# Kernel tuning notes

Measured on AMD Instinct MI355X. Metric: run time of the kernel, lower is better.

Reference implementation:

```python
import jax, jax.numpy as jnp
import numpy as np

LEAKY_SLOPE = 0.2

def _xavier(key, shape, gain=1.414):
    a = gain * np.sqrt(6.0 / (shape[0] + shape[1]))
    return jax.random.uniform(key, shape, minval=-a, maxval=a, dtype=jnp.float32)

C_IN, HID = 64, 128
S_SCALES = [25, 12, 5]
T_SCALES = [64, 32, 16]

def setup_inputs() -> dict:
    key = jax.random.key(0)
    ks = jax.random.split(key, 32)
    B, T, J = 256, 64, 25
    d = {}
    d["src"] = jax.random.normal(ks[0], (B, C_IN, T, J), dtype=jnp.float32)
    d["W"] = _xavier(ks[1], (C_IN, HID))
    for i in range(3):
        d[f"as_src{i}"] = _xavier(ks[2 + i], (HID, 1))
        d[f"as_dst{i}"] = _xavier(ks[5 + i], (HID, 1))
        d[f"at_src{i}"] = _xavier(ks[8 + i], (HID, 1))
        d[f"at_dst{i}"] = _xavier(ks[11 + i], (HID, 1))
    # DiffPool assignment linears: in_features -> next_scale
    d["Wsp0"] = _xavier(ks[14], (C_IN, S_SCALES[1])); d["bsp0"] = jnp.zeros((S_SCALES[1],), jnp.float32)
    d["Wsp1"] = _xavier(ks[15], (C_IN, S_SCALES[2])); d["bsp1"] = jnp.zeros((S_SCALES[2],), jnp.float32)
    d["Wtp0"] = _xavier(ks[16], (C_IN, T_SCALES[1])); d["btp0"] = jnp.zeros((T_SCALES[1],), jnp.float32)
    d["Wtp1"] = _xavier(ks[17], (C_IN, T_SCALES[2])); d["btp1"] = jnp.zeros((T_SCALES[2],), jnp.float32)
    return d


def _gat_attn(emb, a_src, a_dst):
    # emb: [N, n, H]; additive GAT scores -> [N, n, n]
    s = emb @ a_src            # [N, n, 1]
    t = emb @ a_dst            # [N, n, 1]
    return jax.nn.leaky_relu(s + jnp.swapaxes(t, -1, -2), LEAKY_SLOPE)


def _diffpool(x, attn, Wp, bp):
    # assignment S = softmax(Linear(A @ X)) : [N, n, n_next]
    S = jax.nn.softmax((attn @ x) @ Wp + bp, axis=-1)
    x_next = jnp.einsum('bnk,bnc->bkc', S, x)
    return x_next, S


def _branch(x0, W, a_srcs, a_dsts, pool_params):
    n_scales = len(a_srcs)
    attns, pools = [], []
    x_cur = x0
    for i in range(n_scales):
        emb = x_cur @ W
        attns.append(_gat_attn(emb, a_srcs[i], a_dsts[i]))
        if i < n_scales - 1:
            Wp, bp = pool_params[i]
            x_cur, S = _diffpool(x_cur, attns[i], Wp, bp)
            pools.append(S)
    fusion = attns[0]
    for i in range(1, n_scales):
        S = pools[0]
        for j in range(1, i):
            S = S @ pools[j]
        fusion = fusion + S @ attns[i] @ jnp.swapaxes(S, -1, -2)
    # dropout is identity in eval mode
    return jax.nn.softmax(fusion, axis=-1)


def reference(src, W, as_src0, as_src1, as_src2, as_dst0, as_dst1, as_dst2,
              at_src0, at_src1, at_src2, at_dst0, at_dst1, at_dst2,
              Wsp0, bsp0, Wsp1, bsp1, Wtp0, btp0, Wtp1, btp1):
    B, C_in, T, J = src.shape
    x = jnp.transpose(src, (0, 2, 3, 1))              # [B, T, J, C]
    sp_x = x.reshape(B * T, J, C_in)                   # spatial graphs
    tp_x = jnp.transpose(x, (0, 2, 1, 3)).reshape(B * J, T, C_in)  # temporal graphs

    sa = _branch(sp_x, W, [as_src0, as_src1, as_src2], [as_dst0, as_dst1, as_dst2],
                 [(Wsp0, bsp0), (Wsp1, bsp1)])
    ta = _branch(tp_x, W, [at_src0, at_src1, at_src2], [at_dst0, at_dst1, at_dst2],
                 [(Wtp0, btp0), (Wtp1, btp1)])
    return sa.reshape(B, T, J, J), ta.reshape(B, J, T, T)
```

## Files before the change

### kernel.cpp

```cpp
#include <hip/hip_runtime.h>
#include <math.h>

constexpr float LEAKY = 0.2f;

__device__ __forceinline__ float4 ldf4(const float* p){ return *reinterpret_cast<const float4*>(p); }
__device__ __forceinline__ void stf4(float* p, float4 v){ *reinterpret_cast<float4*>(p) = v; }
__device__ __forceinline__ float dot4(float4 a, float4 b){ return a.x*b.x + a.y*b.y + a.z*b.z + a.w*b.w; }
__device__ __forceinline__ float4 fma4(float s, float4 b, float4 acc){
    acc.x += s*b.x; acc.y += s*b.y; acc.z += s*b.z; acc.w += s*b.w; return acc;
}
__device__ __forceinline__ float lrelu(float f){ return f > 0.f ? f : LEAKY*f; }
__device__ __forceinline__ float4 lrelu4(float s, float4 t){
    float4 r; r.x = lrelu(s+t.x); r.y = lrelu(s+t.y); r.z = lrelu(s+t.z); r.w = lrelu(s+t.w); return r;
}
__device__ __forceinline__ float vmax4(float4 v){ return fmaxf(fmaxf(v.x,v.y), fmaxf(v.z,v.w)); }
__device__ __forceinline__ float vsum4(float4 v){ return v.x+v.y+v.z+v.w; }
__device__ __forceinline__ float4 exp4(float4 a, float mx){
    float4 r; r.x = __expf(a.x-mx); r.y = __expf(a.y-mx); r.z = __expf(a.z-mx); r.w = __expf(a.w-mx); return r;
}

__global__ void prep_kernel(const float* __restrict__ W,
    const float* a0, const float* a1, const float* a2,  const float* a3,
    const float* a4, const float* a5, const float* a6,  const float* a7,
    const float* a8, const float* a9, const float* a10, const float* a11,
    const float* __restrict__ Wsp0, const float* __restrict__ Wsp1,
    const float* __restrict__ Wtp0, const float* __restrict__ Wtp1,
    float* __restrict__ ws)
{
    int blk = blockIdx.x, t = threadIdx.x;
    if (blk < 12) {
        const float* as[12] = {a0,a1,a2,a3,a4,a5,a6,a7,a8,a9,a10,a11};
        const float* a = as[blk];
        float s = 0.f;
        #pragma unroll
        for (int h = 0; h < 128; ++h) s += W[t*128 + h] * a[h];
        ws[blk*64 + t] = s;
    } else if (blk == 12) {
        for (int i = t; i < 768; i += 64) { int k = i >> 6, c = i & 63; ws[768 + i] = Wsp0[c*12 + k]; }
    } else if (blk == 13) {
        for (int i = t; i < 320; i += 64) { int k = i >> 6, c = i & 63; ws[1536 + i] = Wsp1[c*5 + k]; }
    } else if (blk == 14) {
        for (int i = t; i < 2048; i += 64) { int k = i >> 6, c = i & 63; ws[1856 + i] = Wtp0[c*32 + k]; }
    } else {
        for (int i = t; i < 1024; i += 64) { int k = i >> 6, c = i & 63; ws[3904 + i] = Wtp1[c*16 + k]; }
    }
}

__global__ __launch_bounds__(512, 4)
void temporal_kernel(const float* __restrict__ src, const float* __restrict__ wvec_g,
                     const float* __restrict__ Wp0, const float* __restrict__ b0,
                     const float* __restrict__ Wp1, const float* __restrict__ b1,
                     float* __restrict__ out, int nwg8)
{
    constexpr int NT = 512;
    constexpr int oA1 = 0;
    constexpr int oP1 = 1152;
    constexpr int oS1 = 1792;

    __shared__ __align__(16) float xr[4352];
    __shared__ __align__(16) float A0[4352];
    __shared__ __align__(16) float PR[2304];
    __shared__ __align__(16) float S0[2304];
    __shared__ __align__(16) float sv[64], tv[64], rx[64], rs[64];
    __shared__ __align__(16) float wv[384];

    const int tid = threadIdx.x;
    const int g = (blockIdx.x & 7) * nwg8 + (blockIdx.x >> 3);
    const int b = g / 25, inner = g - b*25;

    for (int i = tid; i < 384; i += NT) wv[i] = wvec_g[i];
    for (int i = tid; i < 4096; i += NT) {
        int c = i >> 6, r = i & 63;
        xr[r*68 + c] = src[((size_t)(b*64 + c)*64 + r)*25 + inner];
    }
    __syncthreads();

    for (int i = tid; i < 128; i += NT) {
        int which = i >> 6, p = i & 63;
        const float* w = wv + which*64;
        float acc = 0.f;
        #pragma unroll
        for (int c = 0; c < 64; c += 4) acc += dot4(ldf4(&xr[p*68 + c]), ldf4(&w[c]));
        if (which) tv[p] = acc; else sv[p] = acc;
    }
    for (int i = tid; i < 512; i += NT) {
        int p = i >> 3, k4 = i & 7;
        float4 acc = {0,0,0,0};
        #pragma unroll
        for (int c = 0; c < 64; ++c) acc = fma4(xr[p*68 + c], ldf4(&Wp0[c*32 + 4*k4]), acc);
        stf4(&PR[p*36 + 4*k4], acc);
    }
    __syncthreads();

    for (int i = tid; i < 1024; i += NT) {
        int p = i >> 4, q4 = i & 15;
        stf4(&A0[p*68 + 4*q4], lrelu4(sv[p], ldf4(&tv[4*q4])));
    }
    __syncthreads();

    if (tid < 256) {
        int p = tid >> 2, k8 = tid & 3;
        float4 acc0 = ldf4(&b0[8*k8]);
        float4 acc1 = ldf4(&b0[8*k8 + 4]);
        #pragma unroll
        for (int m = 0; m < 64; ++m) {
            float a = A0[p*68 + m];
            acc0 = fma4(a, ldf4(&PR[m*36 + 8*k8]), acc0);
            acc1 = fma4(a, ldf4(&PR[m*36 + 8*k8 + 4]), acc1);
        }
        stf4(&S0[p*36 + 8*k8], acc0);
        stf4(&S0[p*36 + 8*k8 + 4], acc1);
    }
    __syncthreads();

    {
        int p = tid >> 3, l = tid & 7;
        float4 v = ldf4(&S0[p*36 + 4*l]);
        float mx = vmax4(v);
        mx = fmaxf(mx, __shfl_xor(mx,1)); mx = fmaxf(mx, __shfl_xor(mx,2)); mx = fmaxf(mx, __shfl_xor(mx,4));
        v = exp4(v, mx);
        float sm = vsum4(v);
        sm += __shfl_xor(sm,1); sm += __shfl_xor(sm,2); sm += __shfl_xor(sm,4);
        float inv = 1.f/sm;
        v.x *= inv; v.y *= inv; v.z *= inv; v.w *= inv;
        stf4(&S0[p*36 + 4*l], v);
    }
    __syncthreads();

    if (tid < 256) {
        int k = tid >> 3, c8 = tid & 7;
        float4 acc0 = {0,0,0,0}, acc1 = {0,0,0,0};
        #pragma unroll
        for (int p = 0; p < 64; ++p) {
            float s = S0[p*36 + k];
            acc0 = fma4(s, ldf4(&xr[p*68 + 8*c8]), acc0);
            acc1 = fma4(s, ldf4(&xr[p*68 + 8*c8 + 4]), acc1);
        }
        stf4(&PR[k*68 + 8*c8], acc0);
        stf4(&PR[k*68 + 8*c8 + 4], acc1);
    }
    __syncthreads();

    for (int i = tid; i < 64; i += NT) {
        int which = i >> 5, p = i & 31;
        const float* w = wv + (2 + which)*64;
        float acc = 0.f;
        #pragma unroll
        for (int c = 0; c < 64; c += 4) acc += dot4(ldf4(&PR[p*68 + c]), ldf4(&w[c]));
        if (which) tv[p] = acc; else sv[p] = acc;
    }
    for (int i = tid; i < 128; i += NT) {
        int p = i >> 2, k4 = i & 3;
        float4 acc = {0,0,0,0};
        #pragma unroll
        for (int c = 0; c < 64; ++c) acc = fma4(PR[p*68 + c], ldf4(&Wp1[c*16 + 4*k4]), acc);
        stf4(&xr[oP1 + p*20 + 4*k4], acc);
    }
    __syncthreads();

    for (int i = tid; i < 1024; i += NT) {
        int p = i >> 5, q = i & 31;
        xr[oA1 + p*36 + q] = lrelu(sv[p] + tv[q]);
    }
    __syncthreads();

    for (int i = tid; i < 128; i += NT) {
        int p = i >> 2, k4 = i & 3;
        float4 acc = ldf4(&b1[4*k4]);
        #pragma unroll
        for (int m = 0; m < 32; ++m) acc = fma4(xr[oA1 + p*36 + m], ldf4(&xr[oP1 + m*20 + 4*k4]), acc);
        stf4(&xr[oS1 + p*20 + 4*k4], acc);
    }
    __syncthreads();

    if (tid < 128) {
        int m = tid >> 2, l = tid & 3;
        float4 v = ldf4(&xr[oS1 + m*20 + 4*l]);
        float mx = vmax4(v);
        mx = fmaxf(mx, __shfl_xor(mx,1)); mx = fmaxf(mx, __shfl_xor(mx,2));
        v = exp4(v, mx);
        float sm = vsum4(v);
        sm += __shfl_xor(sm,1); sm += __shfl_xor(sm,2);
        float inv = 1.f/sm;
        v.x *= inv; v.y *= inv; v.z *= inv; v.w *= inv;
        stf4(&xr[oS1 + m*20 + 4*l], v);
    } else if (tid < 192) {
        int i = tid - 128;
        int which = i >> 5, p = i & 31;
        const float* w = wv + (4 + which)*64;
        float acc = 0.f;
        #pragma unroll
        for (int c = 0; c < 64; c += 4) acc += dot4(ldf4(&PR[p*68 + c]), ldf4(&w[c]));
        if (which) tv[p] = acc; else sv[p] = acc;
    }
    __syncthreads();

    for (int k = tid; k < 16; k += NT) {
        float a = 0.f, c2 = 0.f;
        #pragma unroll
        for (int n = 0; n < 32; ++n) { float s1 = xr[oS1 + n*20 + k]; a += s1*sv[n]; c2 += s1*tv[n]; }
        rx[k] = a; rs[k] = c2;
    }
    __syncthreads();

    {
        int m = tid >> 4, k = tid & 15;
        float rsk = rs[k];
        float acc = 0.f;
        #pragma unroll
        for (int j = 0; j < 16; ++j)
            acc += xr[oS1 + m*20 + j] * lrelu(rx[j] + rsk);
        xr[oP1 + m*20 + k] = acc;
    }
    __syncthreads();

    for (int i = tid; i < 1024; i += NT) {
        int m = i >> 5, n = i & 31;
        float acc = xr[oA1 + m*36 + n];
        #pragma unroll
        for (int j4 = 0; j4 < 4; ++j4)
            acc += dot4(ldf4(&xr[oP1 + m*20 + 4*j4]), ldf4(&xr[oS1 + n*20 + 4*j4]));
        xr[oA1 + m*36 + n] = acc;
    }
    __syncthreads();

    for (int i = tid; i < 512; i += NT) {
        int p = i >> 3, k4 = i & 7;
        float4 acc = {0,0,0,0};
        #pragma unroll
        for (int m = 0; m < 32; ++m) acc = fma4(S0[p*36 + m], ldf4(&xr[oA1 + m*36 + 4*k4]), acc);
        stf4(&PR[p*36 + 4*k4], acc);
    }
    __syncthreads();

    {
        int q = tid & 63, pg = tid >> 6;
        float4 s0r[8];
        #pragma unroll
        for (int j = 0; j < 8; ++j) s0r[j] = ldf4(&S0[q*36 + 4*j]);
        #pragma unroll
        for (int pi = 0; pi < 8; ++pi) {
            int p = pg*8 + pi;
            float acc = 0.f;
            #pragma unroll
            for (int j = 0; j < 8; ++j) acc += dot4(ldf4(&PR[p*36 + 4*j]), s0r[j]);
            A0[p*68 + q] += acc;
        }
    }
    __syncthreads();

    {
        int p = tid >> 3, l = tid & 7;
        float4 v1 = ldf4(&A0[p*68 + 4*l]);
        float4 v2 = ldf4(&A0[p*68 + 32 + 4*l]);
        float mx = fmaxf(vmax4(v1), vmax4(v2));
        mx = fmaxf(mx, __shfl_xor(mx,1)); mx = fmaxf(mx, __shfl_xor(mx,2)); mx = fmaxf(mx, __shfl_xor(mx,4));
        float4 e1 = exp4(v1, mx), e2 = exp4(v2, mx);
        float sm = vsum4(e1) + vsum4(e2);
        sm += __shfl_xor(sm,1); sm += __shfl_xor(sm,2); sm += __shfl_xor(sm,4);
        float inv = 1.f/sm;
        e1.x*=inv; e1.y*=inv; e1.z*=inv; e1.w*=inv;
        e2.x*=inv; e2.y*=inv; e2.z*=inv; e2.w*=inv;
        size_t base = (size_t)g*4096 + (size_t)p*64;
        stf4(&out[base + 4*l], e1);
        stf4(&out[base + 32 + 4*l], e2);
    }
}

__global__ __launch_bounds__(256, 4)
void spatial_kernel(const float* __restrict__ src, const float* __restrict__ wvg,
                    const float* __restrict__ WpT0, const float* __restrict__ WpT1,
                    const float* __restrict__ b0, const float* __restrict__ b1,
                    float* __restrict__ out, int nwg8)
{
    __shared__ __align__(16) float Rx0[1700];
    __shared__ __align__(16) float RA0[700];
    __shared__ __align__(16) float RPR[816];
    __shared__ __align__(16) float RS0[500];
    __shared__ __align__(16) float sv[32], tv[32], ua[32], va[32], rxa[8], rsa[8];

    float* x0  = Rx0;
    float* A1  = Rx0;
    float* A1T = Rx0 + 240;
    float* P1T = Rx0 + 480;
    float* S1  = Rx0 + 540;
    float* S1T = Rx0 + 684;
    float* A2T = Rx0 + 744;
    float* S01 = Rx0 + 804;
    float* A0  = RA0;
    float* P0T = RPR;
    float* x1  = RPR;
    float* M1  = RPR;
    float* M2  = RPR;
    float* S0  = RS0;

    const int t = threadIdx.x;
    const int g = (blockIdx.x & 7) * nwg8 + (blockIdx.x >> 3);
    const int b = g >> 6, inner = g & 63;
    const float* srcb = src + (size_t)b*102400 + inner*25;

    for (int i = t; i < 400; i += 256) {
        int r = i % 25, c0 = (i / 25) << 2;
        float4 v;
        v.x = srcb[(c0+0)*1600 + r];
        v.y = srcb[(c0+1)*1600 + r];
        v.z = srcb[(c0+2)*1600 + r];
        v.w = srcb[(c0+3)*1600 + r];
        stf4(&x0[r*68 + c0], v);
    }
    __syncthreads();

    if (t < 50) {
        int which = t / 25, p = t - which*25;
        const float* w = wvg + which*64;
        float a = 0.f;
        #pragma unroll
        for (int c4 = 0; c4 < 16; ++c4) a += dot4(ldf4(&x0[p*68 + 4*c4]), ldf4(&w[4*c4]));
        if (which) tv[p] = a; else sv[p] = a;
    }
    for (int i = t; i < 336; i += 256) {
        int k = i / 28, m = i - k*28;
        float a = 0.f;
        if (m < 25) {
            #pragma unroll
            for (int c4 = 0; c4 < 16; ++c4) a += dot4(ldf4(&WpT0[k*64 + 4*c4]), ldf4(&x0[m*68 + 4*c4]));
        }
        P0T[k*28 + m] = a;
    }
    __syncthreads();

    for (int i = t; i < 700; i += 256) {
        int p = i / 28, q = i - p*28;
        A0[i] = (q < 25) ? lrelu(sv[p] + tv[q]) : -1e30f;
    }
    __syncthreads();

    for (int i = t; i < 300; i += 256) {
        int p = i / 12, k = i - p*12;
        float acc = b0[k];
        #pragma unroll
        for (int m4 = 0; m4 < 7; ++m4) acc += dot4(ldf4(&A0[p*28 + 4*m4]), ldf4(&P0T[k*28 + 4*m4]));
        S0[p*20 + k] = acc;
    }
    __syncthreads();

    if (t < 25) {
        float4 r[3]; float mx = -1e30f;
        #pragma unroll
        for (int u = 0; u < 3; ++u) { r[u] = ldf4(&S0[t*20 + 4*u]); mx = fmaxf(mx, vmax4(r[u])); }
        float sm = 0.f;
        #pragma unroll
        for (int u = 0; u < 3; ++u) { r[u] = exp4(r[u], mx); sm += vsum4(r[u]); }
        float inv = 1.f/sm;
        #pragma unroll
        for (int u = 0; u < 3; ++u) {
            r[u].x *= inv; r[u].y *= inv; r[u].z *= inv; r[u].w *= inv;
            stf4(&S0[t*20 + 4*u], r[u]);
        }
    }
    __syncthreads();

    if (t < 96) {
        int k = t >> 3, c0 = (t & 7) << 3;
        float4 a = {0,0,0,0}, bb = {0,0,0,0};
        #pragma unroll
        for (int p = 0; p < 25; ++p) {
            float s = S0[p*20 + k];
            a  = fma4(s, ldf4(&x0[p*68 + c0]), a);
            bb = fma4(s, ldf4(&x0[p*68 + c0 + 4]), bb);
        }
        stf4(&x1[k*68 + c0], a);
        stf4(&x1[k*68 + c0 + 4], bb);
    }
    __syncthreads();

    if (t < 48) {
        int which = t / 12, p = t - which*12;
        const float* w = wvg + (2+which)*64;
        float a = 0.f;
        #pragma unroll
        for (int c4 = 0; c4 < 16; ++c4) a += dot4(ldf4(&x1[p*68 + 4*c4]), ldf4(&w[4*c4]));
        if (which == 0) sv[p] = a; else if (which == 1) tv[p] = a;
        else if (which == 2) ua[p] = a; else va[p] = a;
    }
    for (int i = t; i < 60; i += 256) {
        int j = i / 12, k = i - j*12;
        float a = 0.f;
        #pragma unroll
        for (int c4 = 0; c4 < 16; ++c4) a += dot4(ldf4(&WpT1[j*64 + 4*c4]), ldf4(&x1[k*68 + 4*c4]));
        P1T[j*12 + k] = a;
    }
    __syncthreads();

    for (int i = t; i < 288; i += 256) {
        int mat = i / 144, rr = (i - mat*144) / 12, q = i % 12;
        if (mat == 0) A1 [rr*20 + q] = lrelu(sv[rr] + tv[q]);
        else          A1T[rr*20 + q] = lrelu(sv[q] + tv[rr]);
    }
    __syncthreads();

    for (int i = t; i < 300; i += 256) {
        int p = i / 12, k = i - p*12;
        float acc = 0.f;
        #pragma unroll
        for (int m4 = 0; m4 < 3; ++m4) acc += dot4(ldf4(&S0[p*20 + 4*m4]), ldf4(&A1T[k*20 + 4*m4]));
        M1[p*20 + k] = acc;
    }
    for (int i = t; i < 60; i += 256) {
        int m = i / 5, j = i - m*5;
        float acc = b1[j];
        #pragma unroll
        for (int k4 = 0; k4 < 3; ++k4) acc += dot4(ldf4(&A1[m*20 + 4*k4]), ldf4(&P1T[j*12 + 4*k4]));
        S1[m*12 + j] = acc;
    }
    __syncthreads();

    if (t < 12) {
        float mx = -1e30f;
        float r0 = S1[t*12+0], r1 = S1[t*12+1], r2 = S1[t*12+2], r3 = S1[t*12+3], r4 = S1[t*12+4];
        mx = fmaxf(fmaxf(fmaxf(r0,r1), fmaxf(r2,r3)), r4);
        r0 = __expf(r0-mx); r1 = __expf(r1-mx); r2 = __expf(r2-mx); r3 = __expf(r3-mx); r4 = __expf(r4-mx);
        float inv = 1.f/(r0+r1+r2+r3+r4);
        S1[t*12+0] = r0*inv; S1[t*12+1] = r1*inv; S1[t*12+2] = r2*inv; S1[t*12+3] = r3*inv; S1[t*12+4] = r4*inv;
    }
    for (int i = t; i < 625; i += 256) {
        int p = i / 25, q = i - p*25;
        float acc = A0[p*28 + q];
        #pragma unroll
        for (int m4 = 0; m4 < 3; ++m4) acc += dot4(ldf4(&M1[p*20 + 4*m4]), ldf4(&S0[q*20 + 4*m4]));
        A0[p*28 + q] = acc;
    }
    __syncthreads();

    for (int i = t; i < 60; i += 256) {
        int j = i / 12, m = i - j*12;
        S1T[j*12 + m] = S1[m*12 + j];
    }
    if (t >= 64 && t < 74) {
        int tp = t - 64, which = tp / 5, k = tp - which*5;
        float a = 0.f;
        #pragma unroll
        for (int n = 0; n < 12; ++n) a += S1[n*12 + k] * (which ? va[n] : ua[n]);
        if (which) rsa[k] = a; else rxa[k] = a;
    }
    __syncthreads();

    for (int i = t; i < 40; i += 256) {
        int q = i >> 3, p = i & 7;
        A2T[q*12 + p] = (p < 5) ? lrelu(rxa[p] + rsa[q]) : 0.f;
    }
    for (int i = t; i < 200; i += 256) {
        int p = i >> 3, c = i & 7;
        float acc = 0.f;
        if (c < 5) {
            #pragma unroll
            for (int m4 = 0; m4 < 3; ++m4) acc += dot4(ldf4(&S0[p*20 + 4*m4]), ldf4(&S1T[c*12 + 4*m4]));
        }
        S01[p*12 + c] = acc;
    }
    __syncthreads();

    for (int i = t; i < 200; i += 256) {
        int p = i >> 3, k = i & 7;
        float acc = 0.f;
        if (k < 5) {
            #pragma unroll
            for (int m4 = 0; m4 < 2; ++m4) acc += dot4(ldf4(&S01[p*12 + 4*m4]), ldf4(&A2T[k*12 + 4*m4]));
        }
        M2[p*12 + k] = acc;
    }
    __syncthreads();

    for (int i = t; i < 625; i += 256) {
        int p = i / 25, q = i - p*25;
        float acc = A0[p*28 + q];
        #pragma unroll
        for (int m4 = 0; m4 < 2; ++m4) acc += dot4(ldf4(&M2[p*12 + 4*m4]), ldf4(&S01[q*12 + 4*m4]));
        A0[p*28 + q] = acc;
    }
    __syncthreads();

    if (t < 25) {
        float4 r[7]; float mx = -1e30f;
        #pragma unroll
        for (int u = 0; u < 7; ++u) { r[u] = ldf4(&A0[t*28 + 4*u]); mx = fmaxf(mx, vmax4(r[u])); }
        float sm = 0.f;
        #pragma unroll
        for (int u = 0; u < 7; ++u) sm += vsum4(exp4(r[u], mx));
        sv[t] = mx; tv[t] = 1.f/sm;
    }
    __syncthreads();

    for (int i = t; i < 625; i += 256) {
        int p = i / 25, q = i - p*25;
        out[(size_t)g*625 + i] = __expf(A0[p*28 + q] - sv[p]) * tv[p];
    }
}

extern "C" void kernel_launch(void* const* d_in, const int* in_sizes, int n_in,
                              void* d_out, int out_size, void* d_ws, size_t ws_size,
                              hipStream_t stream) {
    const float* src = (const float*)d_in[0];
    const float* W   = (const float*)d_in[1];
    float* ws = (float*)d_ws;

    prep_kernel<<<16, 64, 0, stream>>>(W,
        (const float*)d_in[2],  (const float*)d_in[3],
        (const float*)d_in[6],  (const float*)d_in[7],
        (const float*)d_in[10], (const float*)d_in[11],
        (const float*)d_in[4],  (const float*)d_in[5],
        (const float*)d_in[8],  (const float*)d_in[9],
        (const float*)d_in[12], (const float*)d_in[13],
        (const float*)d_in[14], (const float*)d_in[16],
        (const float*)d_in[18], (const float*)d_in[20],
        ws);

    float* out = (float*)d_out;
    spatial_kernel<<<16384, 256, 0, stream>>>(
        src, ws, ws + 768, ws + 1536,
        (const float*)d_in[15], (const float*)d_in[17],
        out, 16384/8);
    temporal_kernel<<<6400, 512, 0, stream>>>(
        src, ws + 384,
        (const float*)d_in[18], (const float*)d_in[19],
        (const float*)d_in[20], (const float*)d_in[21],
        out + 10240000, 6400/8);
}
```

Measured before the change: 482.8 us.

## Reassociate pooled projections and fold scale-2 attention into scale-1 term

In the temporal kernel, the pooled-feature products (S^T X)·W and (S^T X)·Wp1 are reassociated as S^T·(X·W) and S^T·(X·Wp1), so the 32x64 pooled feature matrix is never built. The S0 matmul is also register-blocked to two rows per thread. In the spatial kernel, the scale-2 contribution S1·A2·S1^T is added into A1 before projecting through S0, which removes the S01/M2 passes and one 625-element accumulation sweep. These changes cut arithmetic and shared-memory traffic, at the cost of extra shared buffers, added barriers in the spatial path, and slightly different floating-point rounding.

```diff
diff --git a/kernel.cpp b/kernel.cpp
--- a/kernel.cpp
+++ b/kernel.cpp
@@ -61,7 +61,10 @@
     __shared__ __align__(16) float A0[4352];
     __shared__ __align__(16) float PR[2304];
     __shared__ __align__(16) float S0[2304];
+    __shared__ __align__(16) float P01[1280];
+    __shared__ __align__(16) float dv[256];
     __shared__ __align__(16) float sv[64], tv[64], rx[64], rs[64];
+    __shared__ __align__(16) float ua[32], va[32];
     __shared__ __align__(16) float wv[384];
 
     const int tid = threadIdx.x;
@@ -75,20 +78,41 @@
     }
     __syncthreads();
 
-    for (int i = tid; i < 128; i += NT) {
+    for (int i = tid; i < 384; i += NT) {
         int which = i >> 6, p = i & 63;
         const float* w = wv + which*64;
         float acc = 0.f;
         #pragma unroll
-        for (int c = 0; c < 64; c += 4) acc += dot4(ldf4(&xr[p*68 + c]), ldf4(&w[c]));
-        if (which) tv[p] = acc; else sv[p] = acc;
+        for (int c4 = 0; c4 < 16; ++c4) acc += dot4(ldf4(&xr[p*68 + 4*c4]), ldf4(&w[4*c4]));
+        if (which == 0) sv[p] = acc;
+        else if (which == 1) tv[p] = acc;
+        else dv[(which-2)*64 + p] = acc;
     }
     for (int i = tid; i < 512; i += NT) {
         int p = i >> 3, k4 = i & 7;
         float4 acc = {0,0,0,0};
         #pragma unroll
-        for (int c = 0; c < 64; ++c) acc = fma4(xr[p*68 + c], ldf4(&Wp0[c*32 + 4*k4]), acc);
+        for (int c4 = 0; c4 < 16; ++c4) {
+            float4 xv = ldf4(&xr[p*68 + 4*c4]);
+            acc = fma4(xv.x, ldf4(&Wp0[(4*c4+0)*32 + 4*k4]), acc);
+            acc = fma4(xv.y, ldf4(&Wp0[(4*c4+1)*32 + 4*k4]), acc);
+            acc = fma4(xv.z, ldf4(&Wp0[(4*c4+2)*32 + 4*k4]), acc);
+            acc = fma4(xv.w, ldf4(&Wp0[(4*c4+3)*32 + 4*k4]), acc);
+        }
         stf4(&PR[p*36 + 4*k4], acc);
+    }
+    for (int i = tid; i < 256; i += NT) {
+        int p = i >> 2, k4 = i & 3;
+        float4 acc = {0,0,0,0};
+        #pragma unroll
+        for (int c4 = 0; c4 < 16; ++c4) {
+            float4 xv = ldf4(&xr[p*68 + 4*c4]);
+            acc = fma4(xv.x, ldf4(&Wp1[(4*c4+0)*16 + 4*k4]), acc);
+            acc = fma4(xv.y, ldf4(&Wp1[(4*c4+1)*16 + 4*k4]), acc);
+            acc = fma4(xv.z, ldf4(&Wp1[(4*c4+2)*16 + 4*k4]), acc);
+            acc = fma4(xv.w, ldf4(&Wp1[(4*c4+3)*16 + 4*k4]), acc);
+        }
+        stf4(&P01[p*20 + 4*k4], acc);
     }
     __syncthreads();
 
@@ -98,18 +122,26 @@
     }
     __syncthreads();
 
-    if (tid < 256) {
-        int p = tid >> 2, k8 = tid & 3;
-        float4 acc0 = ldf4(&b0[8*k8]);
-        float4 acc1 = ldf4(&b0[8*k8 + 4]);
-        #pragma unroll
-        for (int m = 0; m < 64; ++m) {
-            float a = A0[p*68 + m];
-            acc0 = fma4(a, ldf4(&PR[m*36 + 8*k8]), acc0);
-            acc1 = fma4(a, ldf4(&PR[m*36 + 8*k8 + 4]), acc1);
-        }
-        stf4(&S0[p*36 + 8*k8], acc0);
-        stf4(&S0[p*36 + 8*k8 + 4], acc1);
+    if (tid < 128) {
+        int p0 = tid >> 2, k8 = tid & 3;
+        float4 a00 = ldf4(&b0[8*k8]), a01 = ldf4(&b0[8*k8 + 4]);
+        float4 a10 = a00, a11 = a01;
+        #pragma unroll
+        for (int m4 = 0; m4 < 16; ++m4) {
+            float4 av0 = ldf4(&A0[p0*68 + 4*m4]);
+            float4 av1 = ldf4(&A0[(p0+32)*68 + 4*m4]);
+            const float* f0 = (const float*)&av0;
+            const float* f1 = (const float*)&av1;
+            #pragma unroll
+            for (int j = 0; j < 4; ++j) {
+                float4 pr0 = ldf4(&PR[(4*m4+j)*36 + 8*k8]);
+                float4 pr1 = ldf4(&PR[(4*m4+j)*36 + 8*k8 + 4]);
+                a00 = fma4(f0[j], pr0, a00); a01 = fma4(f0[j], pr1, a01);
+                a10 = fma4(f1[j], pr0, a10); a11 = fma4(f1[j], pr1, a11);
+            }
+        }
+        stf4(&S0[p0*36 + 8*k8], a00);      stf4(&S0[p0*36 + 8*k8 + 4], a01);
+        stf4(&S0[(p0+32)*36 + 8*k8], a10); stf4(&S0[(p0+32)*36 + 8*k8 + 4], a11);
     }
     __syncthreads();
 
@@ -127,34 +159,22 @@
     }
     __syncthreads();
 
-    if (tid < 256) {
-        int k = tid >> 3, c8 = tid & 7;
-        float4 acc0 = {0,0,0,0}, acc1 = {0,0,0,0};
-        #pragma unroll
-        for (int p = 0; p < 64; ++p) {
-            float s = S0[p*36 + k];
-            acc0 = fma4(s, ldf4(&xr[p*68 + 8*c8]), acc0);
-            acc1 = fma4(s, ldf4(&xr[p*68 + 8*c8 + 4]), acc1);
-        }
-        stf4(&PR[k*68 + 8*c8], acc0);
-        stf4(&PR[k*68 + 8*c8 + 4], acc1);
-    }
-    __syncthreads();
-
-    for (int i = tid; i < 64; i += NT) {
-        int which = i >> 5, p = i & 31;
-        const float* w = wv + (2 + which)*64;
+    if (tid < 128) {
+        int k = tid >> 2, j4 = tid & 3;
+        float4 acc = {0,0,0,0};
+        #pragma unroll
+        for (int p = 0; p < 64; ++p)
+            acc = fma4(S0[p*36 + k], ldf4(&P01[p*20 + 4*j4]), acc);
+        stf4(&xr[oP1 + k*20 + 4*j4], acc);
+    } else if (tid < 256) {
+        int i = tid - 128;
+        int j = i >> 5, k = i & 31;
+        const float* d = dv + j*64;
         float acc = 0.f;
         #pragma unroll
-        for (int c = 0; c < 64; c += 4) acc += dot4(ldf4(&PR[p*68 + c]), ldf4(&w[c]));
-        if (which) tv[p] = acc; else sv[p] = acc;
-    }
-    for (int i = tid; i < 128; i += NT) {
-        int p = i >> 2, k4 = i & 3;
-        float4 acc = {0,0,0,0};
-        #pragma unroll
-        for (int c = 0; c < 64; ++c) acc = fma4(PR[p*68 + c], ldf4(&Wp1[c*16 + 4*k4]), acc);
-        stf4(&xr[oP1 + p*20 + 4*k4], acc);
+        for (int p = 0; p < 64; ++p) acc += S0[p*36 + k] * d[p];
+        if (j == 0) sv[k] = acc; else if (j == 1) tv[k] = acc;
+        else if (j == 2) ua[k] = acc; else va[k] = acc;
     }
     __syncthreads();
 
@@ -184,21 +204,13 @@
         float inv = 1.f/sm;
         v.x *= inv; v.y *= inv; v.z *= inv; v.w *= inv;
         stf4(&xr[oS1 + m*20 + 4*l], v);
-    } else if (tid < 192) {
-        int i = tid - 128;
-        int which = i >> 5, p = i & 31;
-        const float* w = wv + (4 + which)*64;
-        float acc = 0.f;
-        #pragma unroll
-        for (int c = 0; c < 64; c += 4) acc += dot4(ldf4(&PR[p*68 + c]), ldf4(&w[c]));
-        if (which) tv[p] = acc; else sv[p] = acc;
     }
     __syncthreads();
 
     for (int k = tid; k < 16; k += NT) {
         float a = 0.f, c2 = 0.f;
         #pragma unroll
-        for (int n = 0; n < 32; ++n) { float s1 = xr[oS1 + n*20 + k]; a += s1*sv[n]; c2 += s1*tv[n]; }
+        for (int n = 0; n < 32; ++n) { float s1 = xr[oS1 + n*20 + k]; a += s1*ua[n]; c2 += s1*va[n]; }
         rx[k] = a; rs[k] = c2;
     }
     __syncthreads();
@@ -284,14 +296,11 @@
     float* A1T = Rx0 + 240;
     float* P1T = Rx0 + 480;
     float* S1  = Rx0 + 540;
-    float* S1T = Rx0 + 684;
-    float* A2T = Rx0 + 744;
-    float* S01 = Rx0 + 804;
+    float* T1  = Rx0 + 744;
     float* A0  = RA0;
     float* P0T = RPR;
     float* x1  = RPR;
     float* M1  = RPR;
-    float* M2  = RPR;
     float* S0  = RS0;
 
     const int t = threadIdx.x;
@@ -399,13 +408,6 @@
     }
     __syncthreads();
 
-    for (int i = t; i < 300; i += 256) {
-        int p = i / 12, k = i - p*12;
-        float acc = 0.f;
-        #pragma unroll
-        for (int m4 = 0; m4 < 3; ++m4) acc += dot4(ldf4(&S0[p*20 + 4*m4]), ldf4(&A1T[k*20 + 4*m4]));
-        M1[p*20 + k] = acc;
-    }
     for (int i = t; i < 60; i += 256) {
         int m = i / 5, j = i - m*5;
         float acc = b1[j];
@@ -423,59 +425,51 @@
         float inv = 1.f/(r0+r1+r2+r3+r4);
         S1[t*12+0] = r0*inv; S1[t*12+1] = r1*inv; S1[t*12+2] = r2*inv; S1[t*12+3] = r3*inv; S1[t*12+4] = r4*inv;
     }
+    __syncthreads();
+
+    if (t < 10) {
+        int which = t / 5, k = t - which*5;
+        float a = 0.f;
+        #pragma unroll
+        for (int n = 0; n < 12; ++n) a += S1[n*12 + k] * (which ? va[n] : ua[n]);
+        if (which) rsa[k] = a; else rxa[k] = a;
+    }
+    __syncthreads();
+
+    if (t < 60) {
+        int m = t / 5, k = t - m*5;
+        float rsk = rsa[k];
+        float acc = 0.f;
+        #pragma unroll
+        for (int j = 0; j < 5; ++j) acc += S1[m*12 + j] * lrelu(rxa[j] + rsk);
+        T1[m*5 + k] = acc;
+    }
+    __syncthreads();
+
+    if (t < 144) {
+        int m = t / 12, n = t - m*12;
+        float acc = A1[m*20 + n];
+        #pragma unroll
+        for (int j = 0; j < 5; ++j) acc += T1[m*5 + j] * S1[n*12 + j];
+        A1[m*20 + n] = acc;
+        A1T[n*20 + m] = acc;
+    }
+    __syncthreads();
+
+    for (int i = t; i < 300; i += 256) {
+        int p = i / 12, k = i - p*12;
+        float acc = 0.f;
+        #pragma unroll
+        for (int m4 = 0; m4 < 3; ++m4) acc += dot4(ldf4(&S0[p*20 + 4*m4]), ldf4(&A1T[k*20 + 4*m4]));
+        M1[p*20 + k] = acc;
+    }
+    __syncthreads();
+
     for (int i = t; i < 625; i += 256) {
         int p = i / 25, q = i - p*25;
         float acc = A0[p*28 + q];
         #pragma unroll
         for (int m4 = 0; m4 < 3; ++m4) acc += dot4(ldf4(&M1[p*20 + 4*m4]), ldf4(&S0[q*20 + 4*m4]));
-        A0[p*28 + q] = acc;
-    }
-    __syncthreads();
-
-    for (int i = t; i < 60; i += 256) {
-        int j = i / 12, m = i - j*12;
-        S1T[j*12 + m] = S1[m*12 + j];
-    }
-    if (t >= 64 && t < 74) {
-        int tp = t - 64, which = tp / 5, k = tp - which*5;
-        float a = 0.f;
-        #pragma unroll
-        for (int n = 0; n < 12; ++n) a += S1[n*12 + k] * (which ? va[n] : ua[n]);
-        if (which) rsa[k] = a; else rxa[k] = a;
-    }
-    __syncthreads();
-
-    for (int i = t; i < 40; i += 256) {
-        int q = i >> 3, p = i & 7;
-        A2T[q*12 + p] = (p < 5) ? lrelu(rxa[p] + rsa[q]) : 0.f;
-    }
-    for (int i = t; i < 200; i += 256) {
-        int p = i >> 3, c = i & 7;
-        float acc = 0.f;
-        if (c < 5) {
-            #pragma unroll
-            for (int m4 = 0; m4 < 3; ++m4) acc += dot4(ldf4(&S0[p*20 + 4*m4]), ldf4(&S1T[c*12 + 4*m4]));
-        }
-        S01[p*12 + c] = acc;
-    }
-    __syncthreads();
-
-    for (int i = t; i < 200; i += 256) {
-        int p = i >> 3, k = i & 7;
-        float acc = 0.f;
-        if (k < 5) {
-            #pragma unroll
-            for (int m4 = 0; m4 < 2; ++m4) acc += dot4(ldf4(&S01[p*12 + 4*m4]), ldf4(&A2T[k*12 + 4*m4]));
-        }
-        M2[p*12 + k] = acc;
-    }
-    __syncthreads();
-
-    for (int i = t; i < 625; i += 256) {
-        int p = i / 25, q = i - p*25;
-        float acc = A0[p*28 + q];
-        #pragma unroll
-        for (int m4 = 0; m4 < 2; ++m4) acc += dot4(ldf4(&M2[p*12 + 4*m4]), ldf4(&S01[q*12 + 4*m4]));
         A0[p*28 + q] = acc;
     }
     __syncthreads();
```

Result: faster. 438.9 us (-9.1%).
